# Kernel optimization log

Measured on AMD Instinct MI355X. Metric: run time of the kernel, lower is better.

Reference implementation:

```python
import jax, jax.numpy as jnp
import numpy as np

T = 2048
V = 1024
H = 2048


def setup_inputs() -> dict:
    key = jax.random.key(0)
    ks = jax.random.split(key, 7)
    s_in = 1.0 / np.sqrt(V + H)
    s_out = 1.0 / np.sqrt(2 * H)
    return {
        "Wf_w": jax.random.normal(ks[0], (4 * H, V + H), jnp.float32) * s_in,
        "Wf_b": jnp.zeros((4 * H,), jnp.float32),
        "Wb_w": jax.random.normal(ks[1], (4 * H, V + H), jnp.float32) * s_in,
        "Wb_b": jnp.zeros((4 * H,), jnp.float32),
        "Wo_w": jax.random.normal(ks[2], (V, 2 * H), jnp.float32) * s_out,
        "Wo_b": jnp.zeros((V,), jnp.float32),
        "char_idx": jax.random.randint(ks[3], (T,), 0, V, jnp.int32),
    }


def _lstm_scan(x_seq, W, b, reverse):
    # x_seq: [T, V]; W: [4H, V+H]; b: [4H]
    h0 = jnp.zeros((H,), x_seq.dtype)
    c0 = jnp.zeros((H,), x_seq.dtype)

    def step(carry, xt):
        h, c = carry
        gates = jnp.concatenate([xt, h]) @ W.T + b  # [4H]
        i, f, g, o = jnp.split(gates, 4)
        i = jax.nn.sigmoid(i)
        f = jax.nn.sigmoid(f)
        o = jax.nn.sigmoid(o)
        g = jnp.tanh(g)
        c_new = f * c + i * g
        h_new = o * jnp.tanh(c_new)
        return (h_new, c_new), h_new

    _, hs = jax.lax.scan(step, (h0, c0), x_seq, reverse=reverse)
    return hs  # [T, H], aligned with input time order


def reference(Wf_w, Wf_b, Wb_w, Wb_b, Wo_w, Wo_b, char_idx):
    x = jax.nn.one_hot(char_idx, V, dtype=Wf_w.dtype)  # [T, V]
    hf = _lstm_scan(x, Wf_w, Wf_b, reverse=False)      # forward states
    hb = _lstm_scan(x, Wb_w, Wb_b, reverse=True)       # backward states
    merged = jnp.concatenate([hf, hb], axis=-1)         # [T, 2H]
    out = merged @ Wo_w.T + Wo_b                        # [T, V]
    return out
```

## Files before the change

kernel.cpp:

```cpp
#include <hip/hip_runtime.h>
#include <math.h>

#define TT 2048
#define VV 1024
#define HH 2048
#define SS (VV + HH)

#define NWGD 128
#define BTH  512
#define UPW  16
#define KSL  32
#define KPT  64

static_assert(NWGD * UPW == HH, "unit coverage");
static_assert(UPW * KSL == BTH, "thread coverage");
static_assert(KSL * KPT == HH, "k coverage");

typedef _Float16 half2_t __attribute__((ext_vector_type(2)));
typedef unsigned uint4v  __attribute__((ext_vector_type(4)));

#if defined(__has_builtin)
#if __has_builtin(__builtin_amdgcn_fdot2)
#define FDOT2(w, h, c) __builtin_amdgcn_fdot2((w), (h), (c), false)
#endif
#endif
#ifndef FDOT2
__device__ __forceinline__ float fdot2_asm(half2_t w, half2_t h, float c) {
    float r = c;
    asm volatile("v_dot2_f32_f16 %0, %1, %2, %0" : "+v"(r) : "v"(w), "v"(h));
    return r;
}
#define FDOT2(w, h, c) fdot2_asm((w), (h), (c))
#endif

__device__ __forceinline__ float sigmoidf_(float x) {
    return 1.0f / (1.0f + __expf(-x));
}


__global__ __launch_bounds__(BTH) __attribute__((amdgpu_waves_per_eu(2, 2)))
void lstm_kernel(const float* __restrict__ Wf, const float* __restrict__ bfv,
                 const float* __restrict__ Wb, const float* __restrict__ bbv,
                 const int* __restrict__ cidx,
                 float* __restrict__ hsf, float* __restrict__ hsb,
                 unsigned* __restrict__ mbx)
{
    const int wg   = blockIdx.x;
    const int dir  = wg >> 7;
    const int w    = wg & (NWGD - 1);
    const int tid  = threadIdx.x;
    const int rg   = tid >> 5;
    const int ks   = tid & (KSL - 1);
    const int unit = w * UPW + rg;

    const float* W    = dir ? Wb : Wf;
    const float* bias = dir ? bbv : bfv;
    float* hs         = dir ? hsb : hsf;
    unsigned* mbd     = mbx + (size_t)dir * (2 * NWGD * 16);

    __shared__ unsigned long long hl2_u64[(KSL * 68) / 4];
    __shared__ ushort hstage[UPW];
    __shared__ char force_one_wg[100 * 1024];
    if (tid == 0) ((volatile char*)force_one_wg)[0] = 0;
    ushort* hl2 = (ushort*)hl2_u64;

    half2_t w2[4][KPT / 2];
    #pragma unroll
    for (int j = 0; j < 4; ++j) {
        const float* rbase = W + (size_t)(j * HH + unit) * SS + VV + ks * KPT;
        #pragma unroll
        for (int q = 0; q < KPT / 4; ++q) {
            const float4 wv = *reinterpret_cast<const float4*>(rbase + 4 * q);
            w2[j][2 * q]     = half2_t{(_Float16)wv.x, (_Float16)wv.y};
            w2[j][2 * q + 1] = half2_t{(_Float16)wv.z, (_Float16)wv.w};
        }
    }
    const float b_i = bias[0 * HH + unit];
    const float b_f = bias[1 * HH + unit];
    const float b_g = bias[2 * HH + unit];
    const float b_o = bias[3 * HH + unit];
    float creg = 0.0f;

    for (int i = tid; i < (KSL * 68) / 4; i += BTH) hl2_u64[i] = 0ull;

    float gx0 = 0.f, gx1 = 0.f, gx2 = 0.f, gx3 = 0.f;
    {
        const int tt0 = dir ? (TT - 1) : 0;
        const int xt0 = cidx[tt0];
        if (ks == 0) {
            gx0 = W[(size_t)(0 * HH + unit) * SS + xt0];
            gx1 = W[(size_t)(1 * HH + unit) * SS + xt0];
            gx2 = W[(size_t)(2 * HH + unit) * SS + xt0];
            gx3 = W[(size_t)(3 * HH + unit) * SS + xt0];
        }
    }
    __syncthreads();

    for (int s = 0; s < TT; ++s) {
        const int t = dir ? (TT - 1 - s) : s;

        float ngx0 = 0.f, ngx1 = 0.f, ngx2 = 0.f, ngx3 = 0.f;
        if ((s + 1 < TT) && (ks == 0)) {
            const int xtn = cidx[dir ? (t - 1) : (t + 1)];
            ngx0 = W[(size_t)(0 * HH + unit) * SS + xtn];
            ngx1 = W[(size_t)(1 * HH + unit) * SS + xtn];
            ngx2 = W[(size_t)(2 * HH + unit) * SS + xtn];
            ngx3 = W[(size_t)(3 * HH + unit) * SS + xtn];
        }

        float a0 = 0.f, a1 = 0.f, a2 = 0.f, a3 = 0.f;
        const ushort* hrow = hl2 + ks * 68;
        #pragma unroll
        for (int c = 0; c < KPT / 4; ++c) {
            const unsigned long long hv8 =
                *reinterpret_cast<const unsigned long long*>(hrow + c * 4);
            const half2_t ha = __builtin_bit_cast(half2_t, (unsigned)hv8);
            const half2_t hc = __builtin_bit_cast(half2_t, (unsigned)(hv8 >> 32));
            a0 = FDOT2(w2[0][2 * c], ha, a0); a0 = FDOT2(w2[0][2 * c + 1], hc, a0);
            a1 = FDOT2(w2[1][2 * c], ha, a1); a1 = FDOT2(w2[1][2 * c + 1], hc, a1);
            a2 = FDOT2(w2[2][2 * c], ha, a2); a2 = FDOT2(w2[2][2 * c + 1], hc, a2);
            a3 = FDOT2(w2[3][2 * c], ha, a3); a3 = FDOT2(w2[3][2 * c + 1], hc, a3);
        }

        float sA = (ks & 1) ? a0 : a1, kA = (ks & 1) ? a1 : a0;
        float A  = kA + __shfl_xor(sA, 1, 64);
        float sB = (ks & 1) ? a2 : a3, kB = (ks & 1) ? a3 : a2;
        float B  = kB + __shfl_xor(sB, 1, 64);
        float sC = (ks & 2) ? A : B,  kC = (ks & 2) ? B : A;
        float C  = kC + __shfl_xor(sC, 2, 64);
        C += __shfl_xor(C, 4, 64);
        C += __shfl_xor(C, 8, 64);
        C += __shfl_xor(C, 16, 64);
        const float Cf = __shfl(C, 1, 32);
        const float Cg = __shfl(C, 2, 32);
        const float Co = __shfl(C, 3, 32);

        if (ks == 0) {
            const float gi = sigmoidf_(C  + gx0 + b_i);
            const float gf = sigmoidf_(Cf + gx1 + b_f);
            const float gg = tanhf(Cg + gx2 + b_g);
            const float go = sigmoidf_(Co + gx3 + b_o);
            creg = gf * creg + gi * gg;
            const float hv = go * tanhf(creg);
            hs[(size_t)t * HH + unit] = hv;
            hstage[rg] = __builtin_bit_cast(ushort, (_Float16)hv);
        }
        gx0 = ngx0; gx1 = ngx1; gx2 = ngx2; gx3 = ngx3;

        __syncthreads();

        if (tid < 4) {
            const unsigned w0 = (unsigned)hstage[4 * tid] |
                                ((unsigned)hstage[4 * tid + 1] << 16);
            const unsigned w1 = (unsigned)hstage[4 * tid + 2] |
                                ((unsigned)hstage[4 * tid + 3] << 16);
            const uint4v pv = {w0, w1, 0u, (unsigned)(s + 1)};
            unsigned* dst = mbd + (size_t)(s & 1) * (NWGD * 16) + w * 16 + tid * 4;
            asm volatile("global_store_dwordx4 %0, %1, off sc0 sc1"
                         :: "v"(dst), "v"(pv) : "memory");
        }

        if (s + 1 < TT) {
            const unsigned tag = (unsigned)(s + 1);
            const unsigned* src = mbd + (size_t)(s & 1) * (NWGD * 16)
                                + (tid >> 2) * 16 + (tid & 3) * 4;
            uint4v v;
            for (;;) {
                asm volatile("global_load_dwordx4 %0, %1, off sc0 sc1\n\t"
                             "s_waitcnt vmcnt(0)"
                             : "=&v"(v) : "v"(src) : "memory");
                if (v.w == tag) break;
                __builtin_amdgcn_s_sleep(1);
            }
            const unsigned long long hv8 =
                (unsigned long long)v.x | ((unsigned long long)v.y << 32);
            *reinterpret_cast<unsigned long long*>(
                hl2 + (tid >> 4) * 68 + (tid & 15) * 4) = hv8;
            __syncthreads();
        }
    }
}

__global__ __launch_bounds__(256)
void out_gemm(const float* __restrict__ hsf, const float* __restrict__ hsb,
              const float* __restrict__ Wo, const float* __restrict__ bo,
              float* __restrict__ out)
{
    const int bn = blockIdx.x;
    const int bm = blockIdx.y;
    const int tid = threadIdx.x;
    const int tx = tid & 15, ty = tid >> 4;
    const int t0 = bm * 64, v0 = bn * 64;

    __shared__ float As[32][72];
    __shared__ float Bs[32][72];

    float acc[4][4] = {};

    const int rr = tid >> 2;
    const int kc = tid & 3;

    for (int kb = 0; kb < 2 * HH; kb += 32) {
        {
            const int k = kb + kc * 8;
            const float* asrc = (k < HH) ? (hsf + (size_t)(t0 + rr) * HH + k)
                                         : (hsb + (size_t)(t0 + rr) * HH + (k - HH));
            const float4 a0 = *reinterpret_cast<const float4*>(asrc);
            const float4 a1 = *reinterpret_cast<const float4*>(asrc + 4);
            const int kk = kc * 8;
            As[kk+0][rr]=a0.x; As[kk+1][rr]=a0.y; As[kk+2][rr]=a0.z; As[kk+3][rr]=a0.w;
            As[kk+4][rr]=a1.x; As[kk+5][rr]=a1.y; As[kk+6][rr]=a1.z; As[kk+7][rr]=a1.w;
            const float* bsrc = Wo + (size_t)(v0 + rr) * (2 * HH) + k;
            const float4 b0 = *reinterpret_cast<const float4*>(bsrc);
            const float4 b1 = *reinterpret_cast<const float4*>(bsrc + 4);
            Bs[kk+0][rr]=b0.x; Bs[kk+1][rr]=b0.y; Bs[kk+2][rr]=b0.z; Bs[kk+3][rr]=b0.w;
            Bs[kk+4][rr]=b1.x; Bs[kk+5][rr]=b1.y; Bs[kk+6][rr]=b1.z; Bs[kk+7][rr]=b1.w;
        }
        __syncthreads();
        #pragma unroll 8
        for (int kk = 0; kk < 32; ++kk) {
            const float4 av = *reinterpret_cast<const float4*>(&As[kk][ty * 4]);
            const float4 bv = *reinterpret_cast<const float4*>(&Bs[kk][tx * 4]);
            const float a[4] = {av.x, av.y, av.z, av.w};
            const float b[4] = {bv.x, bv.y, bv.z, bv.w};
            #pragma unroll
            for (int i2 = 0; i2 < 4; ++i2)
                #pragma unroll
                for (int j2 = 0; j2 < 4; ++j2)
                    acc[i2][j2] = fmaf(a[i2], b[j2], acc[i2][j2]);
        }
        __syncthreads();
    }
    #pragma unroll
    for (int i2 = 0; i2 < 4; ++i2) {
        const int t = t0 + ty * 4 + i2;
        #pragma unroll
        for (int j2 = 0; j2 < 4; ++j2) {
            const int v = v0 + tx * 4 + j2;
            out[(size_t)t * VV + v] = acc[i2][j2] + bo[v];
        }
    }
}

extern "C" void kernel_launch(void* const* d_in, const int* in_sizes, int n_in,
                              void* d_out, int out_size, void* d_ws, size_t ws_size,
                              hipStream_t stream)
{
    (void)in_sizes; (void)n_in; (void)out_size; (void)ws_size;

    const float* Wf  = (const float*)d_in[0];
    const float* bfv = (const float*)d_in[1];
    const float* Wb  = (const float*)d_in[2];
    const float* bbv = (const float*)d_in[3];
    const float* Wo  = (const float*)d_in[4];
    const float* bo  = (const float*)d_in[5];
    const int*   cid = (const int*)d_in[6];
    float* out = (float*)d_out;

    unsigned char* ws = (unsigned char*)d_ws;
    unsigned* mbx = (unsigned*)ws;
    float* hsf = (float*)(ws + 65536);
    float* hsb = hsf + (size_t)TT * HH;

    (void)hipMemsetAsync(mbx, 0, 32768, stream);

    lstm_kernel<<<dim3(2 * NWGD), dim3(BTH), 0, stream>>>(Wf, bfv, Wb, bbv, cid,
                                                          hsf, hsb, mbx);
    out_gemm<<<dim3(VV / 64, TT / 64), dim3(256), 0, stream>>>(hsf, hsb, Wo, bo, out);
}
```

Baseline: 5.716 ms.

## Replace per-step barrier with tagged LDS handoff and double-buffer the h tile

Drops the __syncthreads between the gate computation and the mailbox publish. Instead, each unit's lane-0 writes a step-tagged fp16 h value into LDS, and the four publishing threads spin until all tags match. The h tile in LDS becomes double-buffered by step parity, so one barrier per step is enough, and that barrier now waits only on LDS. The next-step input-gate gather is moved to after the mailbox poll. This trades one block barrier per step for LDS spinning, and it relies on the volatile LDS ordering being correct.

```diff
diff --git a/kernel.cpp b/kernel.cpp
--- a/kernel.cpp
+++ b/kernel.cpp
@@ -11,6 +11,9 @@
 #define UPW  16
 #define KSL  32
 #define KPT  64
+
+#define HL2W 68
+#define HL2SZ (KSL * HL2W)
 
 static_assert(NWGD * UPW == HH, "unit coverage");
 static_assert(UPW * KSL == BTH, "thread coverage");
@@ -36,6 +39,8 @@
 __device__ __forceinline__ float sigmoidf_(float x) {
     return 1.0f / (1.0f + __expf(-x));
 }
+
+#define LDS_BARRIER() asm volatile("s_waitcnt lgkmcnt(0)\n\ts_barrier" ::: "memory")
 
 
 __global__ __launch_bounds__(BTH) __attribute__((amdgpu_waves_per_eu(2, 2)))
@@ -58,8 +63,8 @@
     float* hs         = dir ? hsb : hsf;
     unsigned* mbd     = mbx + (size_t)dir * (2 * NWGD * 16);
 
-    __shared__ unsigned long long hl2_u64[(KSL * 68) / 4];
-    __shared__ ushort hstage[UPW];
+    __shared__ unsigned long long hl2_u64[2 * HL2SZ / 4];
+    __shared__ unsigned hstage[UPW];
     __shared__ char force_one_wg[100 * 1024];
     if (tid == 0) ((volatile char*)force_one_wg)[0] = 0;
     ushort* hl2 = (ushort*)hl2_u64;
@@ -81,35 +86,24 @@
     const float b_o = bias[3 * HH + unit];
     float creg = 0.0f;
 
-    for (int i = tid; i < (KSL * 68) / 4; i += BTH) hl2_u64[i] = 0ull;
+    for (int i = tid; i < HL2SZ / 4; i += BTH) hl2_u64[i] = 0ull;
+    if (tid < UPW) hstage[tid] = 0u;
 
     float gx0 = 0.f, gx1 = 0.f, gx2 = 0.f, gx3 = 0.f;
-    {
-        const int tt0 = dir ? (TT - 1) : 0;
-        const int xt0 = cidx[tt0];
-        if (ks == 0) {
-            gx0 = W[(size_t)(0 * HH + unit) * SS + xt0];
-            gx1 = W[(size_t)(1 * HH + unit) * SS + xt0];
-            gx2 = W[(size_t)(2 * HH + unit) * SS + xt0];
-            gx3 = W[(size_t)(3 * HH + unit) * SS + xt0];
-        }
+    if (ks == 0) {
+        const int xt0 = cidx[dir ? (TT - 1) : 0];
+        gx0 = W[(size_t)(0 * HH + unit) * SS + xt0];
+        gx1 = W[(size_t)(1 * HH + unit) * SS + xt0];
+        gx2 = W[(size_t)(2 * HH + unit) * SS + xt0];
+        gx3 = W[(size_t)(3 * HH + unit) * SS + xt0];
     }
     __syncthreads();
 
     for (int s = 0; s < TT; ++s) {
         const int t = dir ? (TT - 1 - s) : s;
 
-        float ngx0 = 0.f, ngx1 = 0.f, ngx2 = 0.f, ngx3 = 0.f;
-        if ((s + 1 < TT) && (ks == 0)) {
-            const int xtn = cidx[dir ? (t - 1) : (t + 1)];
-            ngx0 = W[(size_t)(0 * HH + unit) * SS + xtn];
-            ngx1 = W[(size_t)(1 * HH + unit) * SS + xtn];
-            ngx2 = W[(size_t)(2 * HH + unit) * SS + xtn];
-            ngx3 = W[(size_t)(3 * HH + unit) * SS + xtn];
-        }
-
         float a0 = 0.f, a1 = 0.f, a2 = 0.f, a3 = 0.f;
-        const ushort* hrow = hl2 + ks * 68;
+        const ushort* hrow = hl2 + (s & 1) * HL2SZ + ks * HL2W;
         #pragma unroll
         for (int c = 0; c < KPT / 4; ++c) {
             const unsigned long long hv8 =
@@ -143,18 +137,23 @@
             creg = gf * creg + gi * gg;
             const float hv = go * tanhf(creg);
             hs[(size_t)t * HH + unit] = hv;
-            hstage[rg] = __builtin_bit_cast(ushort, (_Float16)hv);
-        }
-        gx0 = ngx0; gx1 = ngx1; gx2 = ngx2; gx3 = ngx3;
-
-        __syncthreads();
+            const unsigned hbits =
+                (unsigned)__builtin_bit_cast(ushort, (_Float16)hv);
+            ((volatile unsigned*)hstage)[rg] = ((unsigned)(s + 1) << 16) | hbits;
+        }
 
         if (tid < 4) {
-            const unsigned w0 = (unsigned)hstage[4 * tid] |
-                                ((unsigned)hstage[4 * tid + 1] << 16);
-            const unsigned w1 = (unsigned)hstage[4 * tid + 2] |
-                                ((unsigned)hstage[4 * tid + 3] << 16);
-            const uint4v pv = {w0, w1, 0u, (unsigned)(s + 1)};
+            const unsigned tg = ((unsigned)(s + 1)) << 16;
+            volatile unsigned* hp = hstage + 4 * tid;
+            unsigned x0, x1, x2, x3;
+            for (;;) {
+                x0 = hp[0]; x1 = hp[1]; x2 = hp[2]; x3 = hp[3];
+                if ((((x0 ^ tg) | (x1 ^ tg) | (x2 ^ tg) | (x3 ^ tg))
+                     & 0xFFFF0000u) == 0u) break;
+            }
+            const uint4v pv = {(x0 & 0xFFFFu) | (x1 << 16),
+                               (x2 & 0xFFFFu) | (x3 << 16),
+                               0u, (unsigned)(s + 1)};
             unsigned* dst = mbd + (size_t)(s & 1) * (NWGD * 16) + w * 16 + tid * 4;
             asm volatile("global_store_dwordx4 %0, %1, off sc0 sc1"
                          :: "v"(dst), "v"(pv) : "memory");
@@ -174,9 +173,20 @@
             }
             const unsigned long long hv8 =
                 (unsigned long long)v.x | ((unsigned long long)v.y << 32);
+
+            if (ks == 0) {
+                const int xtn = cidx[dir ? (t - 1) : (t + 1)];
+                gx0 = W[(size_t)(0 * HH + unit) * SS + xtn];
+                gx1 = W[(size_t)(1 * HH + unit) * SS + xtn];
+                gx2 = W[(size_t)(2 * HH + unit) * SS + xtn];
+                gx3 = W[(size_t)(3 * HH + unit) * SS + xtn];
+            }
+
             *reinterpret_cast<unsigned long long*>(
-                hl2 + (tid >> 4) * 68 + (tid & 15) * 4) = hv8;
-            __syncthreads();
+                hl2 + ((s + 1) & 1) * HL2SZ + (tid >> 4) * HL2W + (tid & 15) * 4)
+                = hv8;
+
+            LDS_BARRIER();
         }
     }
 }
```

After: 5.763 ms. Within noise of the previous version (+0.8%).
